# Optimization experiments

Measured on AMD Instinct MI355X. Metric: run time of the kernel, lower is better.

Reference implementation:

```python
import jax, jax.numpy as jnp
import numpy as np
import math

BS, QLEN, DIM, NHEADS = 2, 2048, 1024, 16
HEAD = DIM // NHEADS

def linear(x, w, b):
    # torch nn.Linear: y = x @ w.T + b, w: [out, in]
    return x @ w.T + b

def setup_inputs() -> dict:
    key = jax.random.key(0)
    ks = jax.random.split(key, 6)
    s = 1.0 / math.sqrt(DIM)
    return {
        "input": jax.random.normal(ks[0], (BS * QLEN, DIM), jnp.float32),
        "mask": jnp.zeros((BS, 1, 1, QLEN), jnp.float32),
        "q_w": jax.random.normal(ks[1], (DIM, DIM), jnp.float32) * s,
        "q_b": jnp.zeros((DIM,), jnp.float32),
        "k_w": jax.random.normal(ks[2], (DIM, DIM), jnp.float32) * s,
        "k_b": jnp.zeros((DIM,), jnp.float32),
        "v_w": jax.random.normal(ks[3], (DIM, DIM), jnp.float32) * s,
        "v_b": jnp.zeros((DIM,), jnp.float32),
        "o_w": jax.random.normal(ks[4], (DIM, DIM), jnp.float32) * s,
        "o_b": jnp.zeros((DIM,), jnp.float32),
        "bs": BS,
        "qlen": QLEN,
    }

def reference(input, mask, q_w, q_b, k_w, k_b, v_w, v_b, o_w, o_b, bs, qlen):
    dim = input.shape[-1]
    n_heads = NHEADS
    dph = dim // n_heads

    def split_heads(x):  # [bs*qlen, dim] -> [bs, h, qlen, dph]
        return x.reshape(bs, qlen, n_heads, dph).transpose(0, 2, 1, 3)

    q = split_heads(linear(input, q_w, q_b)) * (1.0 / math.sqrt(dph))
    k = split_heads(linear(input, k_w, k_b))
    v = split_heads(linear(input, v_w, v_b))

    scores = jnp.einsum('bhqd,bhkd->bhqk', q, k) + mask
    weights = jax.nn.softmax(scores.astype(jnp.float32), axis=-1).astype(scores.dtype)
    # dropout: eval mode (training=False) -> identity
    context = jnp.einsum('bhqk,bhkd->bhqd', weights, v)
    context = context.transpose(0, 2, 1, 3).reshape(bs * qlen, dim)
    return linear(context, o_w, o_b)
```

## Files before the change

### kernel.cpp

```cpp
#include <hip/hip_runtime.h>
#include <hip/hip_bf16.h>

typedef __bf16 bf16;
typedef __attribute__((ext_vector_type(8))) __bf16 bf16x8;
typedef __attribute__((ext_vector_type(4))) __bf16 bf16x4;
typedef __attribute__((ext_vector_type(4))) float f32x4;

#define GLOAD_LDS16(g, l) __builtin_amdgcn_global_load_lds( \
    (const __attribute__((address_space(1))) void*)(g),     \
    (__attribute__((address_space(3))) void*)(l), 16, 0, 0)

#if __has_builtin(__builtin_amdgcn_exp2f)
#define EXP2F(x) __builtin_amdgcn_exp2f(x)
#else
#define EXP2F(x) exp2f(x)
#endif

constexpr int MTOT = 4096;
constexpr int DIMC = 1024;
constexpr int QL   = 2048;
constexpr int NH   = 16;
constexpr int HD   = 64;
constexpr float LOG2E = 1.44269504088896340736f;

__global__ __launch_bounds__(256) void prep_cvt(
    const float* __restrict__ x,  const float* __restrict__ qw,
    const float* __restrict__ kw, const float* __restrict__ vw,
    const float* __restrict__ ow, const float* __restrict__ mask,
    bf16* __restrict__ Xb, bf16* __restrict__ Wq, bf16* __restrict__ Wk,
    bf16* __restrict__ Wv, bf16* __restrict__ Wo, bf16* __restrict__ Mexp)
{
  const long long bid = blockIdx.x;
  if (bid >= 8192) {
    const int off = (int)(bid - 8192) * 1024 + threadIdx.x * 4;
    float4 f = *reinterpret_cast<const float4*>(mask + off);
    bf16x4 v;
    v[0] = (bf16)exp2f(f.x * LOG2E); v[1] = (bf16)exp2f(f.y * LOG2E);
    v[2] = (bf16)exp2f(f.z * LOG2E); v[3] = (bf16)exp2f(f.w * LOG2E);
    *reinterpret_cast<bf16x4*>(Mexp + off) = v;
    return;
  }
  const long long i = (bid * 256 + threadIdx.x) * 4;
  const long long nX = (long long)MTOT * DIMC;
  const long long nW = (long long)DIMC * DIMC;
  const float* src; bf16* dst; long long off;
  if      (i < nX)          { src = x;  dst = Xb; off = i; }
  else if (i < nX + nW)     { src = qw; dst = Wq; off = i - nX; }
  else if (i < nX + 2*nW)   { src = kw; dst = Wk; off = i - nX - nW; }
  else if (i < nX + 3*nW)   { src = vw; dst = Wv; off = i - nX - 2*nW; }
  else                      { src = ow; dst = Wo; off = i - nX - 3*nW; }
  float4 f = *reinterpret_cast<const float4*>(src + off);
  bf16x4 v;
  v[0] = (bf16)f.x; v[1] = (bf16)f.y; v[2] = (bf16)f.z; v[3] = (bf16)f.w;
  *reinterpret_cast<bf16x4*>(dst + off) = v;
}

__global__ __launch_bounds__(256) void gemm_bt(
    const bf16* __restrict__ A,
    const bf16* __restrict__ W0, const bf16* __restrict__ W1, const bf16* __restrict__ W2,
    const float* __restrict__ b0, const float* __restrict__ b1, const float* __restrict__ b2,
    bf16* __restrict__ D0, bf16* __restrict__ D1,
    bf16* __restrict__ VtOut, const bf16* __restrict__ Mexp, float scale0)
{
  __shared__ __align__(16) bf16 SMEM[16384];
  bf16* As = SMEM;
  bf16* Bs = SMEM + 8192;

  const bf16* Bm; const float* bias; bf16* D = nullptr; float scale = 1.f;
  const int z = blockIdx.z;
  if (z == 0)      { Bm = W0; bias = b0; D = D0; scale = scale0; }
  else if (z == 1) { Bm = W1; bias = b1; D = D1; }
  else             { Bm = W2; bias = b2; }

  const int tid  = threadIdx.x;
  const int w    = tid >> 6, lane = tid & 63;
  const int gm0  = blockIdx.x * 128, gn0 = blockIdx.y * 128;
  const int wr   = (w >> 1) * 64, wc = (w & 1) * 64;
  const int lr   = lane & 15;
  const int lkB  = (lane >> 4) * 16;
  const int srow = (w << 3) + (lane >> 3);
  const int scolE = (((lane & 7) * 16) ^ ((lane >> 3) << 4)) >> 1;

  f32x4 acc[4][4] = {};

  for (int kt = 0; kt < DIMC / 64; ++kt) {
    __syncthreads();
    const int k0 = kt * 64;
#pragma unroll
    for (int p = 0; p < 4; ++p) {
      const int r = p * 32 + srow;
      GLOAD_LDS16(A  + (size_t)(gm0 + r) * DIMC + k0 + scolE, &As[(p * 32 + (w << 3)) * 64]);
      GLOAD_LDS16(Bm + (size_t)(gn0 + r) * DIMC + k0 + scolE, &Bs[(p * 32 + (w << 3)) * 64]);
    }
    asm volatile("s_waitcnt vmcnt(0)" ::: "memory");
    __syncthreads();

#pragma unroll
    for (int kk = 0; kk < 2; ++kk) {
      bf16x8 af[4], bfv[4];
#pragma unroll
      for (int mf = 0; mf < 4; ++mf) {
        const int r = wr + mf * 16 + lr;
        const int cE = ((kk * 64 + lkB) ^ ((r & 7) << 4)) >> 1;
        af[mf] = *reinterpret_cast<const bf16x8*>(&As[r * 64 + cE]);
      }
#pragma unroll
      for (int nf = 0; nf < 4; ++nf) {
        const int r = wc + nf * 16 + lr;
        const int cE = ((kk * 64 + lkB) ^ ((r & 7) << 4)) >> 1;
        bfv[nf] = *reinterpret_cast<const bf16x8*>(&Bs[r * 64 + cE]);
      }
#pragma unroll
      for (int mf = 0; mf < 4; ++mf)
#pragma unroll
        for (int nf = 0; nf < 4; ++nf)
          acc[mf][nf] = __builtin_amdgcn_mfma_f32_16x16x32_bf16(af[mf], bfv[nf], acc[mf][nf], 0, 0, 0);
    }
  }

  const int orow = (lane >> 4) * 4;

  if (z == 2) {
    bf16* T = SMEM;
    __syncthreads();
#pragma unroll
    for (int mf = 0; mf < 4; ++mf) {
#pragma unroll
      for (int nf = 0; nf < 4; ++nf) {
        const int cl = wc + nf * 16 + lr;
        const float bv = bias[gn0 + cl];
        const int xx = (cl & 7) << 3;
#pragma unroll
        for (int i = 0; i < 4; ++i) {
          const int rl = wr + mf * 16 + orow + i;
          T[cl * 128 + (rl ^ xx)] = (bf16)(acc[mf][nf][i] + bv);
        }
      }
    }
    __syncthreads();
    const int c   = tid >> 1;
    const int rh  = (tid & 1) << 6;
    const int xx2 = (c & 7) << 3;
    const int cg  = gn0 + c;
    const int bb  = gm0 >> 11;
    const int kvb = gm0 & 2047;
    bf16* vtrow = VtOut + (((size_t)bb * 16 + (cg >> 6)) * 64 + (cg & 63)) * (size_t)QL
                  + kvb + rh;
    const bf16* mrow = Mexp + (size_t)bb * QL + kvb + rh;
    const int st = (c >> 3) & 7;
#pragma unroll
    for (int j = 0; j < 8; ++j) {
      const int jj = (j + st) & 7;
      bf16x8 vv = *reinterpret_cast<const bf16x8*>(&T[c * 128 + ((rh + jj * 8) ^ xx2)]);
      const bf16x8 me = *reinterpret_cast<const bf16x8*>(mrow + jj * 8);
#pragma unroll
      for (int e = 0; e < 8; ++e) vv[e] = (bf16)((float)vv[e] * (float)me[e]);
      *reinterpret_cast<bf16x8*>(vtrow + jj * 8) = vv;
    }
    return;
  }

#pragma unroll
  for (int mf = 0; mf < 4; ++mf) {
#pragma unroll
    for (int nf = 0; nf < 4; ++nf) {
      const int c = gn0 + wc + nf * 16 + lr;
      const float bv = bias[c];
#pragma unroll
      for (int i = 0; i < 4; ++i) {
        const int r = gm0 + wr + mf * 16 + orow + i;
        D[(size_t)r * DIMC + c] = (bf16)((acc[mf][nf][i] + bv) * scale);
      }
    }
  }
}

__global__ __launch_bounds__(256) void gemm_o(
    const bf16* __restrict__ A, const bf16* __restrict__ W,
    const float* __restrict__ bias, float* __restrict__ out)
{
  __shared__ __align__(16) bf16 As[128 * 64];
  __shared__ __align__(16) bf16 Bs[64 * 64];

  const int tid  = threadIdx.x;
  const int w    = tid >> 6, lane = tid & 63;
  const int gm0  = blockIdx.x * 128, gn0 = blockIdx.y * 64;
  const int wr   = (w >> 1) * 64, wc = (w & 1) * 32;
  const int lr   = lane & 15;
  const int lkB  = (lane >> 4) * 16;
  const int srow = (w << 3) + (lane >> 3);
  const int scolE = (((lane & 7) * 16) ^ ((lane >> 3) << 4)) >> 1;

  f32x4 acc[4][2] = {};

  for (int kt = 0; kt < DIMC / 64; ++kt) {
    __syncthreads();
    const int k0 = kt * 64;
#pragma unroll
    for (int p = 0; p < 4; ++p) {
      const int r = p * 32 + srow;
      GLOAD_LDS16(A + (size_t)(gm0 + r) * DIMC + k0 + scolE, &As[(p * 32 + (w << 3)) * 64]);
    }
#pragma unroll
    for (int p = 0; p < 2; ++p) {
      const int r = p * 32 + srow;
      GLOAD_LDS16(W + (size_t)(gn0 + r) * DIMC + k0 + scolE, &Bs[(p * 32 + (w << 3)) * 64]);
    }
    asm volatile("s_waitcnt vmcnt(0)" ::: "memory");
    __syncthreads();

#pragma unroll
    for (int kk = 0; kk < 2; ++kk) {
      bf16x8 af[4], bfv[2];
#pragma unroll
      for (int mf = 0; mf < 4; ++mf) {
        const int r = wr + mf * 16 + lr;
        const int cE = ((kk * 64 + lkB) ^ ((r & 7) << 4)) >> 1;
        af[mf] = *reinterpret_cast<const bf16x8*>(&As[r * 64 + cE]);
      }
#pragma unroll
      for (int nf = 0; nf < 2; ++nf) {
        const int r = wc + nf * 16 + lr;
        const int cE = ((kk * 64 + lkB) ^ ((r & 7) << 4)) >> 1;
        bfv[nf] = *reinterpret_cast<const bf16x8*>(&Bs[r * 64 + cE]);
      }
#pragma unroll
      for (int mf = 0; mf < 4; ++mf)
#pragma unroll
        for (int nf = 0; nf < 2; ++nf)
          acc[mf][nf] = __builtin_amdgcn_mfma_f32_16x16x32_bf16(af[mf], bfv[nf], acc[mf][nf], 0, 0, 0);
    }
  }

  const int orow = (lane >> 4) * 4;
#pragma unroll
  for (int mf = 0; mf < 4; ++mf) {
#pragma unroll
    for (int nf = 0; nf < 2; ++nf) {
      const int c = gn0 + wc + nf * 16 + lr;
      const float bv = bias[c];
#pragma unroll
      for (int i = 0; i < 4; ++i) {
        const int r = gm0 + wr + mf * 16 + orow + i;
        out[(size_t)r * DIMC + c] = acc[mf][nf][i] + bv;
      }
    }
  }
}

__global__ __launch_bounds__(512, 4) void attn_fwd(
    const bf16* __restrict__ Q, const bf16* __restrict__ K, const bf16* __restrict__ Vt,
    const bf16* __restrict__ Mexp, bf16* __restrict__ ctx)
{
  __shared__ __align__(16) bf16 Kls[4 * 4096];
  __shared__ __align__(16) bf16 Vls[4 * 4096];
  __shared__ __align__(16) bf16 Ps[8][16 * 36];

  const int tid = threadIdx.x, w = tid >> 6, lane = tid & 63;
  const int bid = blockIdx.x;
  const int logical = (bid & 7) * 64 + (bid >> 3);
  const int qt = logical & 15, bh = logical >> 4;
  const int b = bh >> 4, h = bh & 15;
  const size_t rowbase = (size_t)b * QL;
  const int lr = lane & 15, g = lane >> 4;
  const int lkB = g * 16;

  bf16x8 aq[2];
  {
    const bf16* qp = Q + (rowbase + qt * 128 + w * 16 + lr) * DIMC + h * HD + g * 8;
    aq[0] = *reinterpret_cast<const bf16x8*>(qp);
    aq[1] = *reinterpret_cast<const bf16x8*>(qp + 32);
  }

  const int g_row  = tid >> 3;
  const int g_colE = (((tid & 7) * 16) ^ ((g_row & 7) << 4)) >> 1;
  const bf16* Kt0 = K  + rowbase * DIMC + h * HD;
  const bf16* Vt0 = Vt + (size_t)bh * HD * QL;
  const bf16* MexpP = Mexp + rowbase;

#define ATTN_STAGE(tt, bb) do {                                               \
    GLOAD_LDS16(Kt0 + (size_t)((tt) * 64 + g_row) * DIMC + g_colE,            \
                &Kls[(bb) * 4096 + tid * 8]);                                 \
    GLOAD_LDS16(Vt0 + (size_t)g_row * QL + (tt) * 64 + g_colE,                \
                &Vls[(bb) * 4096 + tid * 8]);                                 \
  } while (0)

  const f32x4 zf4 = {0.f, 0.f, 0.f, 0.f};

#define QK_COMPUTE(TT, SACC) do {                                             \
    const bf16* Kb = &Kls[((TT) % 4) * 4096];                                 \
    bf16x8 bk0[4], bk1[4];                                                    \
    _Pragma("unroll")                                                         \
    for (int nf = 0; nf < 4; ++nf) {                                          \
      const int r = nf * 16 + lr;                                             \
      const int c0 = ((lkB)      ^ ((r & 7) << 4)) >> 1;                      \
      const int c1 = ((64 + lkB) ^ ((r & 7) << 4)) >> 1;                      \
      bk0[nf] = *reinterpret_cast<const bf16x8*>(&Kb[r * 64 + c0]);           \
      bk1[nf] = *reinterpret_cast<const bf16x8*>(&Kb[r * 64 + c1]);           \
    }                                                                         \
    __builtin_amdgcn_s_setprio(1);                                            \
    _Pragma("unroll")                                                         \
    for (int nf = 0; nf < 4; ++nf)                                            \
      SACC[nf] = __builtin_amdgcn_mfma_f32_16x16x32_bf16(bk0[nf], aq[0], zf4, 0, 0, 0); \
    _Pragma("unroll")                                                         \
    for (int nf = 0; nf < 4; ++nf)                                            \
      SACC[nf] = __builtin_amdgcn_mfma_f32_16x16x32_bf16(bk1[nf], aq[1], SACC[nf], 0, 0, 0); \
    __builtin_amdgcn_s_setprio(0);                                            \
  } while (0)

#define SM_PV_HALF(TT, SC, HALF) do {                                         \
    _Pragma("unroll")                                                         \
    for (int nn = 0; nn < 2; ++nn) {                                          \
      const int nf = (HALF) * 2 + nn;                                         \
      const float p0 = EXP2F(SC[nf][0]);                                      \
      const float p1 = EXP2F(SC[nf][1]);                                      \
      const float p2 = EXP2F(SC[nf][2]);                                      \
      const float p3 = EXP2F(SC[nf][3]);                                      \
      bf16x4 pv;                                                              \
      pv[0] = (bf16)p0; pv[1] = (bf16)p1; pv[2] = (bf16)p2; pv[3] = (bf16)p3; \
      *reinterpret_cast<bf16x4*>(&Ps[w][lr * 36 + nn * 16 + g * 4]) = pv;     \
    }                                                                         \
    const bf16x4 lo = *reinterpret_cast<const bf16x4*>(&Ps[w][lr * 36 + g * 8]);     \
    const bf16x4 hi = *reinterpret_cast<const bf16x4*>(&Ps[w][lr * 36 + g * 8 + 4]); \
    bf16x8 ap;                                                                \
    _Pragma("unroll")                                                         \
    for (int j = 0; j < 4; ++j) { ap[j] = lo[j]; ap[4 + j] = hi[j]; }         \
    const bf16x8 mfrag = *reinterpret_cast<const bf16x8*>(                    \
        MexpP + (TT) * 64 + (HALF) * 32 + g * 8);                             \
    const bf16* Vb = &Vls[((TT) % 4) * 4096];                                 \
    bf16x8 bv[4];                                                             \
    _Pragma("unroll")                                                         \
    for (int df = 0; df < 4; ++df) {                                          \
      const int r = df * 16 + lr;                                             \
      const int cE = (((HALF) * 64 + lkB) ^ ((r & 7) << 4)) >> 1;             \
      bv[df] = *reinterpret_cast<const bf16x8*>(&Vb[r * 64 + cE]);            \
    }                                                                         \
    __builtin_amdgcn_s_setprio(1);                                            \
    acc_l = __builtin_amdgcn_mfma_f32_16x16x32_bf16(ap, mfrag, acc_l, 0, 0, 0); \
    _Pragma("unroll")                                                         \
    for (int df = 0; df < 4; ++df)                                            \
      acc_o[df] = __builtin_amdgcn_mfma_f32_16x16x32_bf16(ap, bv[df], acc_o[df], 0, 0, 0); \
    __builtin_amdgcn_s_setprio(0);                                            \
  } while (0)

#define ITER_END() do {                                                       \
    asm volatile("s_waitcnt vmcnt(2) lgkmcnt(0)" ::: "memory");               \
    __builtin_amdgcn_s_barrier();                                             \
    __builtin_amdgcn_sched_barrier(0);                                        \
  } while (0)

  f32x4 acc_l = {};
  f32x4 acc_o[4] = {};
  f32x4 sA[4], sB[4];

  constexpr int NT = QL / 64;

  ATTN_STAGE(0, 0);
  ATTN_STAGE(1, 1);
  ATTN_STAGE(2, 2);
  asm volatile("s_waitcnt vmcnt(4)" ::: "memory");
  __builtin_amdgcn_s_barrier();
  QK_COMPUTE(0, sA);
  ITER_END();

  for (int tt = 0; tt < NT; tt += 2) {
    {
      const int T = tt;
      const int stg = (T + 3 < NT) ? (T + 3) : (NT - 1);
      ATTN_STAGE(stg, (T + 3) & 3);
      QK_COMPUTE(T + 1, sB);
      SM_PV_HALF(T, sA, 0);
      SM_PV_HALF(T, sA, 1);
      ITER_END();
    }
    {
      const int T = tt + 1;
      const int stg = (T + 3 < NT) ? (T + 3) : (NT - 1);
      ATTN_STAGE(stg, (T + 3) & 3);
      if (T + 1 < NT) QK_COMPUTE(T + 1, sA);
      SM_PV_HALF(T, sB, 0);
      SM_PV_HALF(T, sB, 1);
      ITER_END();
    }
  }
#undef ATTN_STAGE
#undef QK_COMPUTE
#undef SM_PV_HALF
#undef ITER_END

#pragma unroll
  for (int i = 0; i < 4; ++i) {
    const float inv = 1.0f / acc_l[i];
    const size_t r = rowbase + qt * 128 + w * 16 + g * 4 + i;
#pragma unroll
    for (int df = 0; df < 4; ++df)
      ctx[r * DIMC + h * HD + df * 16 + lr] = (bf16)(acc_o[df][i] * inv);
  }
}

extern "C" void kernel_launch(void* const* d_in, const int* in_sizes, int n_in,
                              void* d_out, int out_size, void* d_ws, size_t ws_size,
                              hipStream_t stream) {
  const float* x    = (const float*)d_in[0];
  const float* mask = (const float*)d_in[1];
  const float* qw = (const float*)d_in[2]; const float* qb = (const float*)d_in[3];
  const float* kw = (const float*)d_in[4]; const float* kb = (const float*)d_in[5];
  const float* vw = (const float*)d_in[6]; const float* vb = (const float*)d_in[7];
  const float* ow = (const float*)d_in[8]; const float* ob = (const float*)d_in[9];
  float* out = (float*)d_out;

  bf16* Xb  = (bf16*)d_ws;
  bf16* Wqb = Xb  + (size_t)MTOT * DIMC;
  bf16* Wkb = Wqb + (size_t)DIMC * DIMC;
  bf16* Wvb = Wkb + (size_t)DIMC * DIMC;
  bf16* Wob = Wvb + (size_t)DIMC * DIMC;
  bf16* Qb  = Wob + (size_t)DIMC * DIMC;
  bf16* Kb  = Qb  + (size_t)MTOT * DIMC;
  bf16* Cb  = Kb  + (size_t)MTOT * DIMC;
  bf16* Vt  = Cb  + (size_t)MTOT * DIMC;
  bf16* Mex = Vt  + (size_t)MTOT * DIMC;

  prep_cvt<<<8196, 256, 0, stream>>>(x, qw, kw, vw, ow, mask,
                                     Xb, Wqb, Wkb, Wvb, Wob, Mex);

  gemm_bt<<<dim3(32, 8, 3), 256, 0, stream>>>(
      Xb, Wqb, Wkb, Wvb, qb, kb, vb, Qb, Kb, Vt, Mex, 0.125f * LOG2E);

  attn_fwd<<<512, 512, 0, stream>>>(Qb, Kb, Vt, Mex, Cb);

  gemm_o<<<dim3(32, 16), 256, 0, stream>>>(Cb, Wob, ob, out);
}
```

Baseline: 117.8 us.

## Process two query sub-tiles per wave in attention, halve block size; vectorize V-transpose store

The attention kernel now runs 256 threads per block with each wave handling 32 query rows (two 16-row sub-tiles) instead of 16. Each K/V fragment read from LDS therefore feeds twice as many MFMAs, and per-thread global-to-LDS staging doubles to keep the same tile size. The cost is roughly double the accumulator and score registers per wave and fewer waves per block to hide latency. Separately, the V-transpose epilogue in the QKV GEMM writes four bf16 values with one vector store instead of four scalar stores.

```diff
diff --git a/kernel.cpp b/kernel.cpp
--- a/kernel.cpp
+++ b/kernel.cpp
@@ -130,11 +130,11 @@
         const int cl = wc + nf * 16 + lr;
         const float bv = bias[gn0 + cl];
         const int xx = (cl & 7) << 3;
-#pragma unroll
-        for (int i = 0; i < 4; ++i) {
-          const int rl = wr + mf * 16 + orow + i;
-          T[cl * 128 + (rl ^ xx)] = (bf16)(acc[mf][nf][i] + bv);
-        }
+        const int rl0 = wr + mf * 16 + orow;
+        bf16x4 tv;
+#pragma unroll
+        for (int i = 0; i < 4; ++i) tv[i] = (bf16)(acc[mf][nf][i] + bv);
+        *reinterpret_cast<bf16x4*>(&T[cl * 128 + (rl0 ^ xx)]) = tv;
       }
     }
     __syncthreads();
@@ -248,13 +248,13 @@
   }
 }
 
-__global__ __launch_bounds__(512, 4) void attn_fwd(
+__global__ __launch_bounds__(256, 2) void attn_fwd(
     const bf16* __restrict__ Q, const bf16* __restrict__ K, const bf16* __restrict__ Vt,
     const bf16* __restrict__ Mexp, bf16* __restrict__ ctx)
 {
   __shared__ __align__(16) bf16 Kls[4 * 4096];
   __shared__ __align__(16) bf16 Vls[4 * 4096];
-  __shared__ __align__(16) bf16 Ps[8][16 * 36];
+  __shared__ __align__(16) bf16 Ps[4][2 * 16 * 36];
 
   const int tid = threadIdx.x, w = tid >> 6, lane = tid & 63;
   const int bid = blockIdx.x;
@@ -265,30 +265,40 @@
   const int lr = lane & 15, g = lane >> 4;
   const int lkB = g * 16;
 
-  bf16x8 aq[2];
-  {
-    const bf16* qp = Q + (rowbase + qt * 128 + w * 16 + lr) * DIMC + h * HD + g * 8;
-    aq[0] = *reinterpret_cast<const bf16x8*>(qp);
-    aq[1] = *reinterpret_cast<const bf16x8*>(qp + 32);
-  }
-
-  const int g_row  = tid >> 3;
-  const int g_colE = (((tid & 7) * 16) ^ ((g_row & 7) << 4)) >> 1;
+  bf16x8 aq[2][2];
+#pragma unroll
+  for (int s = 0; s < 2; ++s) {
+    const bf16* qp = Q + (rowbase + qt * 128 + w * 32 + s * 16 + lr) * DIMC + h * HD + g * 8;
+    aq[s][0] = *reinterpret_cast<const bf16x8*>(qp);
+    aq[s][1] = *reinterpret_cast<const bf16x8*>(qp + 32);
+  }
+
+  int g_row[2], g_colE[2];
+#pragma unroll
+  for (int s2 = 0; s2 < 2; ++s2) {
+    const int ci = s2 * 256 + tid;
+    const int row = ci >> 3;
+    g_row[s2]  = row;
+    g_colE[s2] = (((ci & 7) * 16) ^ ((row & 7) << 4)) >> 1;
+  }
   const bf16* Kt0 = K  + rowbase * DIMC + h * HD;
   const bf16* Vt0 = Vt + (size_t)bh * HD * QL;
   const bf16* MexpP = Mexp + rowbase;
 
 #define ATTN_STAGE(tt, bb) do {                                               \
-    GLOAD_LDS16(Kt0 + (size_t)((tt) * 64 + g_row) * DIMC + g_colE,            \
-                &Kls[(bb) * 4096 + tid * 8]);                                 \
-    GLOAD_LDS16(Vt0 + (size_t)g_row * QL + (tt) * 64 + g_colE,                \
-                &Vls[(bb) * 4096 + tid * 8]);                                 \
+    _Pragma("unroll")                                                         \
+    for (int s2 = 0; s2 < 2; ++s2) {                                          \
+      GLOAD_LDS16(Kt0 + (size_t)((tt) * 64 + g_row[s2]) * DIMC + g_colE[s2],  \
+                  &Kls[(bb) * 4096 + (s2 * 256 + tid) * 8]);                  \
+      GLOAD_LDS16(Vt0 + (size_t)g_row[s2] * QL + (tt) * 64 + g_colE[s2],      \
+                  &Vls[(bb) * 4096 + (s2 * 256 + tid) * 8]);                  \
+    }                                                                         \
   } while (0)
 
   const f32x4 zf4 = {0.f, 0.f, 0.f, 0.f};
 
 #define QK_COMPUTE(TT, SACC) do {                                             \
-    const bf16* Kb = &Kls[((TT) % 4) * 4096];                                 \
+    const bf16* Kb = &Kls[((TT) & 3) * 4096];                                 \
     bf16x8 bk0[4], bk1[4];                                                    \
     _Pragma("unroll")                                                         \
     for (int nf = 0; nf < 4; ++nf) {                                          \
@@ -300,34 +310,36 @@
     }                                                                         \
     __builtin_amdgcn_s_setprio(1);                                            \
     _Pragma("unroll")                                                         \
-    for (int nf = 0; nf < 4; ++nf)                                            \
-      SACC[nf] = __builtin_amdgcn_mfma_f32_16x16x32_bf16(bk0[nf], aq[0], zf4, 0, 0, 0); \
-    _Pragma("unroll")                                                         \
-    for (int nf = 0; nf < 4; ++nf)                                            \
-      SACC[nf] = __builtin_amdgcn_mfma_f32_16x16x32_bf16(bk1[nf], aq[1], SACC[nf], 0, 0, 0); \
+    for (int s = 0; s < 2; ++s)                                               \
+      _Pragma("unroll")                                                       \
+      for (int nf = 0; nf < 4; ++nf)                                          \
+        SACC[s][nf] = __builtin_amdgcn_mfma_f32_16x16x32_bf16(bk0[nf], aq[s][0], zf4, 0, 0, 0); \
+    _Pragma("unroll")                                                         \
+    for (int s = 0; s < 2; ++s)                                               \
+      _Pragma("unroll")                                                       \
+      for (int nf = 0; nf < 4; ++nf)                                          \
+        SACC[s][nf] = __builtin_amdgcn_mfma_f32_16x16x32_bf16(bk1[nf], aq[s][1], SACC[s][nf], 0, 0, 0); \
     __builtin_amdgcn_s_setprio(0);                                            \
   } while (0)
 
 #define SM_PV_HALF(TT, SC, HALF) do {                                         \
     _Pragma("unroll")                                                         \
-    for (int nn = 0; nn < 2; ++nn) {                                          \
-      const int nf = (HALF) * 2 + nn;                                         \
-      const float p0 = EXP2F(SC[nf][0]);                                      \
-      const float p1 = EXP2F(SC[nf][1]);                                      \
-      const float p2 = EXP2F(SC[nf][2]);                                      \
-      const float p3 = EXP2F(SC[nf][3]);                                      \
-      bf16x4 pv;                                                              \
-      pv[0] = (bf16)p0; pv[1] = (bf16)p1; pv[2] = (bf16)p2; pv[3] = (bf16)p3; \
-      *reinterpret_cast<bf16x4*>(&Ps[w][lr * 36 + nn * 16 + g * 4]) = pv;     \
+    for (int s = 0; s < 2; ++s) {                                             \
+      _Pragma("unroll")                                                       \
+      for (int nn = 0; nn < 2; ++nn) {                                        \
+        const int nf = (HALF) * 2 + nn;                                       \
+        const float p0 = EXP2F(SC[s][nf][0]);                                 \
+        const float p1 = EXP2F(SC[s][nf][1]);                                 \
+        const float p2 = EXP2F(SC[s][nf][2]);                                 \
+        const float p3 = EXP2F(SC[s][nf][3]);                                 \
+        bf16x4 pv;                                                            \
+        pv[0] = (bf16)p0; pv[1] = (bf16)p1; pv[2] = (bf16)p2; pv[3] = (bf16)p3; \
+        *reinterpret_cast<bf16x4*>(&Ps[w][s * 576 + lr * 36 + nn * 16 + g * 4]) = pv; \
+      }                                                                       \
     }                                                                         \
-    const bf16x4 lo = *reinterpret_cast<const bf16x4*>(&Ps[w][lr * 36 + g * 8]);     \
-    const bf16x4 hi = *reinterpret_cast<const bf16x4*>(&Ps[w][lr * 36 + g * 8 + 4]); \
-    bf16x8 ap;                                                                \
-    _Pragma("unroll")                                                         \
-    for (int j = 0; j < 4; ++j) { ap[j] = lo[j]; ap[4 + j] = hi[j]; }         \
     const bf16x8 mfrag = *reinterpret_cast<const bf16x8*>(                    \
         MexpP + (TT) * 64 + (HALF) * 32 + g * 8);                             \
-    const bf16* Vb = &Vls[((TT) % 4) * 4096];                                 \
+    const bf16* Vb = &Vls[((TT) & 3) * 4096];                                 \
     bf16x8 bv[4];                                                             \
     _Pragma("unroll")                                                         \
     for (int df = 0; df < 4; ++df) {                                          \
@@ -335,30 +347,46 @@
       const int cE = (((HALF) * 64 + lkB) ^ ((r & 7) << 4)) >> 1;             \
       bv[df] = *reinterpret_cast<const bf16x8*>(&Vb[r * 64 + cE]);            \
     }                                                                         \
+    bf16x8 ap0, ap1;                                                          \
+    {                                                                         \
+      const bf16x4 lo0 = *reinterpret_cast<const bf16x4*>(&Ps[w][0 * 576 + lr * 36 + g * 8]); \
+      const bf16x4 hi0 = *reinterpret_cast<const bf16x4*>(&Ps[w][0 * 576 + lr * 36 + g * 8 + 4]); \
+      const bf16x4 lo1 = *reinterpret_cast<const bf16x4*>(&Ps[w][1 * 576 + lr * 36 + g * 8]); \
+      const bf16x4 hi1 = *reinterpret_cast<const bf16x4*>(&Ps[w][1 * 576 + lr * 36 + g * 8 + 4]); \
+      _Pragma("unroll")                                                       \
+      for (int j = 0; j < 4; ++j) {                                           \
+        ap0[j] = lo0[j]; ap0[4 + j] = hi0[j];                                 \
+        ap1[j] = lo1[j]; ap1[4 + j] = hi1[j];                                 \
+      }                                                                       \
+    }                                                                         \
     __builtin_amdgcn_s_setprio(1);                                            \
-    acc_l = __builtin_amdgcn_mfma_f32_16x16x32_bf16(ap, mfrag, acc_l, 0, 0, 0); \
+    acc_l[0] = __builtin_amdgcn_mfma_f32_16x16x32_bf16(ap0, mfrag, acc_l[0], 0, 0, 0); \
+    acc_l[1] = __builtin_amdgcn_mfma_f32_16x16x32_bf16(ap1, mfrag, acc_l[1], 0, 0, 0); \
     _Pragma("unroll")                                                         \
     for (int df = 0; df < 4; ++df)                                            \
-      acc_o[df] = __builtin_amdgcn_mfma_f32_16x16x32_bf16(ap, bv[df], acc_o[df], 0, 0, 0); \
+      acc_o[0][df] = __builtin_amdgcn_mfma_f32_16x16x32_bf16(ap0, bv[df], acc_o[0][df], 0, 0, 0); \
+    _Pragma("unroll")                                                         \
+    for (int df = 0; df < 4; ++df)                                            \
+      acc_o[1][df] = __builtin_amdgcn_mfma_f32_16x16x32_bf16(ap1, bv[df], acc_o[1][df], 0, 0, 0); \
     __builtin_amdgcn_s_setprio(0);                                            \
   } while (0)
 
 #define ITER_END() do {                                                       \
-    asm volatile("s_waitcnt vmcnt(2) lgkmcnt(0)" ::: "memory");               \
+    asm volatile("s_waitcnt vmcnt(4) lgkmcnt(0)" ::: "memory");               \
     __builtin_amdgcn_s_barrier();                                             \
     __builtin_amdgcn_sched_barrier(0);                                        \
   } while (0)
 
-  f32x4 acc_l = {};
-  f32x4 acc_o[4] = {};
-  f32x4 sA[4], sB[4];
+  f32x4 acc_l[2] = {};
+  f32x4 acc_o[2][4] = {};
+  f32x4 sA[2][4], sB[2][4];
 
   constexpr int NT = QL / 64;
 
   ATTN_STAGE(0, 0);
   ATTN_STAGE(1, 1);
   ATTN_STAGE(2, 2);
-  asm volatile("s_waitcnt vmcnt(4)" ::: "memory");
+  asm volatile("s_waitcnt vmcnt(8)" ::: "memory");
   __builtin_amdgcn_s_barrier();
   QK_COMPUTE(0, sA);
   ITER_END();
@@ -389,12 +417,15 @@
 #undef ITER_END
 
 #pragma unroll
-  for (int i = 0; i < 4; ++i) {
-    const float inv = 1.0f / acc_l[i];
-    const size_t r = rowbase + qt * 128 + w * 16 + g * 4 + i;
-#pragma unroll
-    for (int df = 0; df < 4; ++df)
-      ctx[r * DIMC + h * HD + df * 16 + lr] = (bf16)(acc_o[df][i] * inv);
+  for (int s = 0; s < 2; ++s) {
+#pragma unroll
+    for (int i = 0; i < 4; ++i) {
+      const float inv = 1.0f / acc_l[s][i];
+      const size_t r = rowbase + qt * 128 + w * 32 + s * 16 + g * 4 + i;
+#pragma unroll
+      for (int df = 0; df < 4; ++df)
+        ctx[r * DIMC + h * HD + df * 16 + lr] = (bf16)(acc_o[s][df][i] * inv);
+    }
   }
 }
 
@@ -426,7 +457,7 @@
   gemm_bt<<<dim3(32, 8, 3), 256, 0, stream>>>(
       Xb, Wqb, Wkb, Wvb, qb, kb, vb, Qb, Kb, Vt, Mex, 0.125f * LOG2E);
 
-  attn_fwd<<<512, 512, 0, stream>>>(Qb, Kb, Vt, Mex, Cb);
+  attn_fwd<<<512, 256, 0, stream>>>(Qb, Kb, Vt, Mex, Cb);
 
   gemm_o<<<dim3(32, 16), 256, 0, stream>>>(Cb, Wob, ob, out);
 }
```

Result: no change. 118.1 us (+0.2%).
